# Kernel optimization log

Measured on AMD Instinct MI355X. Metric: run time of the kernel, lower is better.

Reference implementation:

```python
import jax, jax.numpy as jnp
import numpy as np

EMBED_DIM = 1280
NUM_HEADS = 20
HEAD_DIM = EMBED_DIM // NUM_HEADS
ENC_LEN = 8192
SCALE = float(HEAD_DIM ** -0.5)


def setup_inputs() -> dict:
    key = jax.random.key(0)
    ks = jax.random.split(key, 7)
    s = 0.02
    return {
        "hidden_states": jax.random.normal(ks[0], (1, 1, EMBED_DIM), dtype=jnp.float32),
        "cross_k_cache": jax.random.normal(ks[1], (1, NUM_HEADS, ENC_LEN, HEAD_DIM), dtype=jnp.float32),
        "cross_v_cache": jax.random.normal(ks[2], (1, NUM_HEADS, ENC_LEN, HEAD_DIM), dtype=jnp.float32),
        "q_w": jax.random.normal(ks[3], (EMBED_DIM, EMBED_DIM), dtype=jnp.float32) * s,
        "q_b": jax.random.normal(ks[4], (EMBED_DIM,), dtype=jnp.float32) * s,
        "out_w": jax.random.normal(ks[5], (EMBED_DIM, EMBED_DIM), dtype=jnp.float32) * s,
        "out_b": jax.random.normal(ks[6], (EMBED_DIM,), dtype=jnp.float32) * s,
    }


def reference(hidden_states, cross_k_cache, cross_v_cache, q_w, q_b, out_w, out_b):
    # q_proj (torch Linear: x @ W.T + b), then scale
    q = hidden_states @ q_w.T + q_b                       # [1,1,E]
    q = q * jnp.asarray(SCALE, q.dtype)
    q = q.reshape(1, 1, NUM_HEADS, HEAD_DIM).transpose(0, 2, 1, 3)  # [1,H,1,Dh]
    # attention scores over cached keys: [1,H,1,L]
    attn = jnp.einsum("bhqd,bhld->bhql", q, cross_k_cache)
    attn = jax.nn.softmax(attn, axis=-1)
    # weighted sum of values: [1,H,1,Dh]
    out = jnp.einsum("bhql,bhld->bhqd", attn, cross_v_cache)
    out = out.transpose(0, 2, 1, 3).reshape(1, 1, EMBED_DIM)
    return out @ out_w.T + out_b
```

## Files before the change

kernel.cpp:

```cpp
#include <hip/hip_runtime.h>
#include <math.h>

#define EMBED 1280
#define NHEAD 20
#define HDIM 64
#define LENC 8192
#define CHUNK 128
#define NCHUNK (LENC / CHUNK)
#define PREC 72
#define QSCALE 0.125f

__global__ __launch_bounds__(256) void matvec1280(
    const float* __restrict__ W, const float* __restrict__ x,
    const float* __restrict__ b, float* __restrict__ y, float scale) {
  int j = blockIdx.x * 4 + (threadIdx.x >> 6);
  int lane = threadIdx.x & 63;
  const float4* Wr = reinterpret_cast<const float4*>(W + (size_t)j * EMBED);
  const float4* x4 = reinterpret_cast<const float4*>(x);
  float acc = 0.f;
#pragma unroll
  for (int k = 0; k < 5; ++k) {
    float4 wv = Wr[lane + 64 * k];
    float4 xv = x4[lane + 64 * k];
    acc += wv.x * xv.x + wv.y * xv.y + wv.z * xv.z + wv.w * xv.w;
  }
#pragma unroll
  for (int m = 32; m > 0; m >>= 1) acc += __shfl_xor(acc, m);
  if (lane == 0) y[j] = scale * (acc + b[j]);
}

__global__ __launch_bounds__(256) void attn_partial(
    const float* __restrict__ K, const float* __restrict__ V,
    const float* __restrict__ q, float* __restrict__ part) {
  int blk = blockIdx.x;
  int h = blk / NCHUNK;
  int c = blk % NCHUNK;
  int tid = threadIdx.x;
  int w = tid >> 6;
  int lane = tid & 63;
  int grp = lane >> 4;
  int l16 = lane & 15;

  __shared__ float sc[CHUNK];
  __shared__ float red[8];
  __shared__ float4 ovec[4][16];

  const float4* Kh4 = reinterpret_cast<const float4*>(
      K + (size_t)h * LENC * HDIM + (size_t)c * CHUNK * HDIM);
  const float4* Vh4 = reinterpret_cast<const float4*>(
      V + (size_t)h * LENC * HDIM + (size_t)c * CHUNK * HDIM);
  float4 qv = reinterpret_cast<const float4*>(q + h * HDIM)[l16];

#pragma unroll
  for (int it = 0; it < CHUNK / 16; ++it) {
    int row = w * (CHUNK / 4) + it * 4 + grp;
    float4 kv = Kh4[row * 16 + l16];
    float s = kv.x * qv.x + kv.y * qv.y + kv.z * qv.z + kv.w * qv.w;
    s += __shfl_xor(s, 1);
    s += __shfl_xor(s, 2);
    s += __shfl_xor(s, 4);
    s += __shfl_xor(s, 8);
    if (l16 == 0) sc[row] = s;
  }
  __syncthreads();

  float m = (tid < CHUNK) ? sc[tid] : -INFINITY;
#pragma unroll
  for (int msk = 32; msk > 0; msk >>= 1) m = fmaxf(m, __shfl_xor(m, msk));
  if (lane == 0) red[w] = m;
  __syncthreads();
  float M = fmaxf(fmaxf(red[0], red[1]), fmaxf(red[2], red[3]));

  float e = (tid < CHUNK) ? expf(sc[tid] - M) : 0.f;
  if (tid < CHUNK) sc[tid] = e;
  float ssum = e;
#pragma unroll
  for (int msk = 32; msk > 0; msk >>= 1) ssum += __shfl_xor(ssum, msk);
  if (lane == 0) red[4 + w] = ssum;
  __syncthreads();
  float S = red[4] + red[5] + red[6] + red[7];

  float4 acc = make_float4(0.f, 0.f, 0.f, 0.f);
#pragma unroll
  for (int it = 0; it < CHUNK / 16; ++it) {
    int row = w * (CHUNK / 4) + it * 4 + grp;
    float4 vv = Vh4[row * 16 + l16];
    float p = sc[row];
    acc.x += p * vv.x; acc.y += p * vv.y; acc.z += p * vv.z; acc.w += p * vv.w;
  }
#pragma unroll
  for (int msk = 16; msk <= 32; msk <<= 1) {
    acc.x += __shfl_xor(acc.x, msk);
    acc.y += __shfl_xor(acc.y, msk);
    acc.z += __shfl_xor(acc.z, msk);
    acc.w += __shfl_xor(acc.w, msk);
  }
  if (grp == 0) ovec[w][l16] = acc;
  __syncthreads();

  if (w == 0 && grp == 0) {
    float4 o0 = ovec[0][l16], o1 = ovec[1][l16], o2 = ovec[2][l16], o3 = ovec[3][l16];
    float4 o = make_float4(o0.x + o1.x + o2.x + o3.x, o0.y + o1.y + o2.y + o3.y,
                           o0.z + o1.z + o2.z + o3.z, o0.w + o1.w + o2.w + o3.w);
    float* p = part + (size_t)(h * NCHUNK + c) * PREC;
    if (tid == 0) { p[0] = M; p[1] = S; }
    reinterpret_cast<float4*>(p + 4)[l16] = o;
  }
}

__global__ __launch_bounds__(64) void attn_combine(
    const float* __restrict__ part, float* __restrict__ attn_out) {
  int h = blockIdx.x;
  int lane = threadIdx.x;
  const float* p = part + (size_t)h * NCHUNK * PREC;
  float M = -INFINITY;
#pragma unroll
  for (int c = 0; c < NCHUNK; ++c) M = fmaxf(M, p[c * PREC]);
  float S = 0.f, o = 0.f;
#pragma unroll
  for (int c = 0; c < NCHUNK; ++c) {
    float f = expf(p[c * PREC] - M);
    S += p[c * PREC + 1] * f;
    o += p[c * PREC + 4 + lane] * f;
  }
  attn_out[h * HDIM + lane] = o / S;
}


extern "C" void kernel_launch(void* const* d_in, const int* in_sizes, int n_in,
                              void* d_out, int out_size, void* d_ws, size_t ws_size,
                              hipStream_t stream) {
  const float* hs    = (const float*)d_in[0];
  const float* Kc    = (const float*)d_in[1];
  const float* Vc    = (const float*)d_in[2];
  const float* q_w   = (const float*)d_in[3];
  const float* q_b   = (const float*)d_in[4];
  const float* out_w = (const float*)d_in[5];
  const float* out_b = (const float*)d_in[6];
  float* out = (float*)d_out;

  float* ws = (float*)d_ws;
  float* qv       = ws;
  float* attn_out = ws + EMBED;
  float* part     = ws + 2 * EMBED;

  matvec1280<<<EMBED / 4, 256, 0, stream>>>(q_w, hs, q_b, qv, QSCALE);
  attn_partial<<<NHEAD * NCHUNK, 256, 0, stream>>>(Kc, Vc, qv, part);
  attn_combine<<<NHEAD, 64, 0, stream>>>(part, attn_out);
  matvec1280<<<EMBED / 4, 256, 0, stream>>>(out_w, attn_out, out_b, out, 1.0f);
}
```

Before: 34.39 us.

## Fuse split-softmax combine into attention kernel via last-block atomic counter

Removes the separate combine kernel launch. Each attention block bumps a per-head atomic counter after writing its partial result, and the last block to finish for a head merges all the partials. The counters are zeroed inside the first matvec kernel. The matvec is also restructured to one row per 256-thread block (1280 blocks) with a shared-memory reduction, in place of four rows per block. The price is an atomic and fences per attention block, plus a serialized combine in the final block of each head.

```diff
diff --git a/kernel.cpp b/kernel.cpp
--- a/kernel.cpp
+++ b/kernel.cpp
@@ -10,28 +10,36 @@
 #define PREC 72
 #define QSCALE 0.125f
 
-__global__ __launch_bounds__(256) void matvec1280(
+__global__ __launch_bounds__(256) void matvec_row(
     const float* __restrict__ W, const float* __restrict__ x,
-    const float* __restrict__ b, float* __restrict__ y, float scale) {
-  int j = blockIdx.x * 4 + (threadIdx.x >> 6);
-  int lane = threadIdx.x & 63;
-  const float4* Wr = reinterpret_cast<const float4*>(W + (size_t)j * EMBED);
+    const float* __restrict__ b, float* __restrict__ y, float scale,
+    int* __restrict__ cnt_zero) {
+  if (cnt_zero != nullptr && blockIdx.x < NHEAD && threadIdx.x == 0)
+    __hip_atomic_store(&cnt_zero[blockIdx.x], 0, __ATOMIC_RELEASE,
+                       __HIP_MEMORY_SCOPE_AGENT);
+  int row = blockIdx.x;
+  int t = threadIdx.x;
+  int w = t >> 6, lane = t & 63;
+  const float4* Wr = reinterpret_cast<const float4*>(W + (size_t)row * EMBED);
   const float4* x4 = reinterpret_cast<const float4*>(x);
-  float acc = 0.f;
-#pragma unroll
-  for (int k = 0; k < 5; ++k) {
-    float4 wv = Wr[lane + 64 * k];
-    float4 xv = x4[lane + 64 * k];
-    acc += wv.x * xv.x + wv.y * xv.y + wv.z * xv.z + wv.w * xv.w;
+  float4 wv = Wr[t], xv = x4[t];
+  float acc = wv.x * xv.x + wv.y * xv.y + wv.z * xv.z + wv.w * xv.w;
+  if (t < 64) {
+    float4 wv2 = Wr[256 + t], xv2 = x4[256 + t];
+    acc += wv2.x * xv2.x + wv2.y * xv2.y + wv2.z * xv2.z + wv2.w * xv2.w;
   }
 #pragma unroll
-  for (int m = 32; m > 0; m >>= 1) acc += __shfl_xor(acc, m);
-  if (lane == 0) y[j] = scale * (acc + b[j]);
+  for (int msk = 32; msk > 0; msk >>= 1) acc += __shfl_xor(acc, msk);
+  __shared__ float red[4];
+  if (lane == 0) red[w] = acc;
+  __syncthreads();
+  if (t == 0) y[row] = scale * (red[0] + red[1] + red[2] + red[3] + b[row]);
 }
 
 __global__ __launch_bounds__(256) void attn_partial(
     const float* __restrict__ K, const float* __restrict__ V,
-    const float* __restrict__ q, float* __restrict__ part) {
+    const float* __restrict__ q, float* __restrict__ part,
+    int* __restrict__ cnt, float* __restrict__ attn_out) {
   int blk = blockIdx.x;
   int h = blk / NCHUNK;
   int c = blk % NCHUNK;
@@ -44,6 +52,7 @@
   __shared__ float sc[CHUNK];
   __shared__ float red[8];
   __shared__ float4 ovec[4][16];
+  __shared__ int sWon;
 
   const float4* Kh4 = reinterpret_cast<const float4*>(
       K + (size_t)h * LENC * HDIM + (size_t)c * CHUNK * HDIM);
@@ -106,24 +115,31 @@
     if (tid == 0) { p[0] = M; p[1] = S; }
     reinterpret_cast<float4*>(p + 4)[l16] = o;
   }
-}
+  __syncthreads();
 
-__global__ __launch_bounds__(64) void attn_combine(
-    const float* __restrict__ part, float* __restrict__ attn_out) {
-  int h = blockIdx.x;
-  int lane = threadIdx.x;
-  const float* p = part + (size_t)h * NCHUNK * PREC;
-  float M = -INFINITY;
+  if (tid == 0) {
+    __threadfence();
+    int old = atomicAdd(&cnt[h], 1);
+    sWon = (old == NCHUNK - 1) ? 1 : 0;
+  }
+  __syncthreads();
+  if (sWon) {
+    __threadfence();
+    if (tid < HDIM) {
+      const float* p = part + (size_t)h * NCHUNK * PREC;
+      float Mg = -INFINITY;
 #pragma unroll
-  for (int c = 0; c < NCHUNK; ++c) M = fmaxf(M, p[c * PREC]);
-  float S = 0.f, o = 0.f;
+      for (int cc = 0; cc < NCHUNK; ++cc) Mg = fmaxf(Mg, p[cc * PREC]);
+      float Sg = 0.f, o = 0.f;
 #pragma unroll
-  for (int c = 0; c < NCHUNK; ++c) {
-    float f = expf(p[c * PREC] - M);
-    S += p[c * PREC + 1] * f;
-    o += p[c * PREC + 4 + lane] * f;
+      for (int cc = 0; cc < NCHUNK; ++cc) {
+        float f = expf(p[cc * PREC] - Mg);
+        Sg += p[cc * PREC + 1] * f;
+        o += p[cc * PREC + 4 + tid] * f;
+      }
+      attn_out[h * HDIM + tid] = o / Sg;
+    }
   }
-  attn_out[h * HDIM + lane] = o / S;
 }
 
 
@@ -140,12 +156,12 @@
   float* out = (float*)d_out;
 
   float* ws = (float*)d_ws;
-  float* qv       = ws;
-  float* attn_out = ws + EMBED;
-  float* part     = ws + 2 * EMBED;
+  int*   cnt      = (int*)ws;
+  float* qv       = ws + 32;
+  float* attn_out = ws + 32 + EMBED;
+  float* part     = ws + 32 + 2 * EMBED;
 
-  matvec1280<<<EMBED / 4, 256, 0, stream>>>(q_w, hs, q_b, qv, QSCALE);
-  attn_partial<<<NHEAD * NCHUNK, 256, 0, stream>>>(Kc, Vc, qv, part);
-  attn_combine<<<NHEAD, 64, 0, stream>>>(part, attn_out);
-  matvec1280<<<EMBED / 4, 256, 0, stream>>>(out_w, attn_out, out_b, out, 1.0f);
+  matvec_row<<<EMBED, 256, 0, stream>>>(q_w, hs, q_b, qv, QSCALE, cnt);
+  attn_partial<<<NHEAD * NCHUNK, 256, 0, stream>>>(Kc, Vc, qv, part, cnt, attn_out);
+  matvec_row<<<EMBED, 256, 0, stream>>>(out_w, attn_out, out_b, out, 1.0f, nullptr);
 }
```

Measured after the change: 83.14 us. +141.7%, slower.

## Make attention partials wave-local, preload K/V in registers, parallelize combine

Applied to the files above, without the earlier changes.

The attention partial kernel now has each wavefront do its own 32-row softmax. Each wavefront writes its own partial record (256 records per head), so the block-wide shared-memory reductions and syncthreads are gone. All K and V loads are issued up front into registers to raise memory-level parallelism. The combine kernel uses 256 threads with shared-memory reductions over four times as many records, and the matvec now assigns one row per 256-thread block. The trade-offs are more partial-record traffic, more register pressure, and four times more matvec blocks.

```diff
diff --git a/kernel.cpp b/kernel.cpp
--- a/kernel.cpp
+++ b/kernel.cpp
@@ -6,124 +6,143 @@
 #define HDIM 64
 #define LENC 8192
 #define CHUNK 128
-#define NCHUNK (LENC / CHUNK)
+#define NBLK (LENC / CHUNK)
+#define NREC 256
 #define PREC 72
 #define QSCALE 0.125f
 
-__global__ __launch_bounds__(256) void matvec1280(
+__global__ __launch_bounds__(256) void matvec_row(
     const float* __restrict__ W, const float* __restrict__ x,
     const float* __restrict__ b, float* __restrict__ y, float scale) {
-  int j = blockIdx.x * 4 + (threadIdx.x >> 6);
-  int lane = threadIdx.x & 63;
-  const float4* Wr = reinterpret_cast<const float4*>(W + (size_t)j * EMBED);
+  int row = blockIdx.x;
+  int t = threadIdx.x;
+  int w = t >> 6, lane = t & 63;
+  const float4* Wr = reinterpret_cast<const float4*>(W + (size_t)row * EMBED);
   const float4* x4 = reinterpret_cast<const float4*>(x);
-  float acc = 0.f;
-#pragma unroll
-  for (int k = 0; k < 5; ++k) {
-    float4 wv = Wr[lane + 64 * k];
-    float4 xv = x4[lane + 64 * k];
-    acc += wv.x * xv.x + wv.y * xv.y + wv.z * xv.z + wv.w * xv.w;
+  float4 wv = Wr[t], xv = x4[t];
+  float acc = wv.x * xv.x + wv.y * xv.y + wv.z * xv.z + wv.w * xv.w;
+  if (t < 64) {
+    float4 wv2 = Wr[256 + t], xv2 = x4[256 + t];
+    acc += wv2.x * xv2.x + wv2.y * xv2.y + wv2.z * xv2.z + wv2.w * xv2.w;
   }
 #pragma unroll
-  for (int m = 32; m > 0; m >>= 1) acc += __shfl_xor(acc, m);
-  if (lane == 0) y[j] = scale * (acc + b[j]);
+  for (int msk = 32; msk > 0; msk >>= 1) acc += __shfl_xor(acc, msk);
+  __shared__ float red[4];
+  if (lane == 0) red[w] = acc;
+  __syncthreads();
+  if (t == 0) y[row] = scale * (red[0] + red[1] + red[2] + red[3] + b[row]);
 }
 
 __global__ __launch_bounds__(256) void attn_partial(
     const float* __restrict__ K, const float* __restrict__ V,
     const float* __restrict__ q, float* __restrict__ part) {
   int blk = blockIdx.x;
-  int h = blk / NCHUNK;
-  int c = blk % NCHUNK;
+  int h = blk / NBLK;
+  int c = blk % NBLK;
   int tid = threadIdx.x;
   int w = tid >> 6;
   int lane = tid & 63;
   int grp = lane >> 4;
   int l16 = lane & 15;
 
-  __shared__ float sc[CHUNK];
-  __shared__ float red[8];
-  __shared__ float4 ovec[4][16];
-
-  const float4* Kh4 = reinterpret_cast<const float4*>(
-      K + (size_t)h * LENC * HDIM + (size_t)c * CHUNK * HDIM);
-  const float4* Vh4 = reinterpret_cast<const float4*>(
-      V + (size_t)h * LENC * HDIM + (size_t)c * CHUNK * HDIM);
+  size_t row0 = (size_t)c * CHUNK + (size_t)w * 32;
+  const float4* Kh4 = reinterpret_cast<const float4*>(K + (size_t)h * LENC * HDIM) + row0 * 16;
+  const float4* Vh4 = reinterpret_cast<const float4*>(V + (size_t)h * LENC * HDIM) + row0 * 16;
   float4 qv = reinterpret_cast<const float4*>(q + h * HDIM)[l16];
 
+  float4 kreg[8], vreg[8];
 #pragma unroll
-  for (int it = 0; it < CHUNK / 16; ++it) {
-    int row = w * (CHUNK / 4) + it * 4 + grp;
-    float4 kv = Kh4[row * 16 + l16];
-    float s = kv.x * qv.x + kv.y * qv.y + kv.z * qv.z + kv.w * qv.w;
-    s += __shfl_xor(s, 1);
-    s += __shfl_xor(s, 2);
-    s += __shfl_xor(s, 4);
-    s += __shfl_xor(s, 8);
-    if (l16 == 0) sc[row] = s;
+  for (int it = 0; it < 8; ++it) kreg[it] = Kh4[(it * 4 + grp) * 16 + l16];
+#pragma unroll
+  for (int it = 0; it < 8; ++it) vreg[it] = Vh4[(it * 4 + grp) * 16 + l16];
+
+  float s[8];
+#pragma unroll
+  for (int it = 0; it < 8; ++it) {
+    float t = kreg[it].x * qv.x + kreg[it].y * qv.y + kreg[it].z * qv.z + kreg[it].w * qv.w;
+    t += __shfl_xor(t, 1);
+    t += __shfl_xor(t, 2);
+    t += __shfl_xor(t, 4);
+    t += __shfl_xor(t, 8);
+    s[it] = t;
   }
-  __syncthreads();
 
-  float m = (tid < CHUNK) ? sc[tid] : -INFINITY;
+  float m = s[0];
 #pragma unroll
-  for (int msk = 32; msk > 0; msk >>= 1) m = fmaxf(m, __shfl_xor(m, msk));
-  if (lane == 0) red[w] = m;
-  __syncthreads();
-  float M = fmaxf(fmaxf(red[0], red[1]), fmaxf(red[2], red[3]));
+  for (int it = 1; it < 8; ++it) m = fmaxf(m, s[it]);
+  m = fmaxf(m, __shfl_xor(m, 16));
+  m = fmaxf(m, __shfl_xor(m, 32));
 
-  float e = (tid < CHUNK) ? expf(sc[tid] - M) : 0.f;
-  if (tid < CHUNK) sc[tid] = e;
-  float ssum = e;
+  float e[8], ssum = 0.f;
 #pragma unroll
-  for (int msk = 32; msk > 0; msk >>= 1) ssum += __shfl_xor(ssum, msk);
-  if (lane == 0) red[4 + w] = ssum;
-  __syncthreads();
-  float S = red[4] + red[5] + red[6] + red[7];
+  for (int it = 0; it < 8; ++it) { e[it] = expf(s[it] - m); ssum += e[it]; }
+  ssum += __shfl_xor(ssum, 16);
+  ssum += __shfl_xor(ssum, 32);
 
-  float4 acc = make_float4(0.f, 0.f, 0.f, 0.f);
+  float4 o = make_float4(0.f, 0.f, 0.f, 0.f);
 #pragma unroll
-  for (int it = 0; it < CHUNK / 16; ++it) {
-    int row = w * (CHUNK / 4) + it * 4 + grp;
-    float4 vv = Vh4[row * 16 + l16];
-    float p = sc[row];
-    acc.x += p * vv.x; acc.y += p * vv.y; acc.z += p * vv.z; acc.w += p * vv.w;
+  for (int it = 0; it < 8; ++it) {
+    o.x += e[it] * vreg[it].x;
+    o.y += e[it] * vreg[it].y;
+    o.z += e[it] * vreg[it].z;
+    o.w += e[it] * vreg[it].w;
   }
 #pragma unroll
   for (int msk = 16; msk <= 32; msk <<= 1) {
-    acc.x += __shfl_xor(acc.x, msk);
-    acc.y += __shfl_xor(acc.y, msk);
-    acc.z += __shfl_xor(acc.z, msk);
-    acc.w += __shfl_xor(acc.w, msk);
+    o.x += __shfl_xor(o.x, msk);
+    o.y += __shfl_xor(o.y, msk);
+    o.z += __shfl_xor(o.z, msk);
+    o.w += __shfl_xor(o.w, msk);
   }
-  if (grp == 0) ovec[w][l16] = acc;
-  __syncthreads();
 
-  if (w == 0 && grp == 0) {
-    float4 o0 = ovec[0][l16], o1 = ovec[1][l16], o2 = ovec[2][l16], o3 = ovec[3][l16];
-    float4 o = make_float4(o0.x + o1.x + o2.x + o3.x, o0.y + o1.y + o2.y + o3.y,
-                           o0.z + o1.z + o2.z + o3.z, o0.w + o1.w + o2.w + o3.w);
-    float* p = part + (size_t)(h * NCHUNK + c) * PREC;
-    if (tid == 0) { p[0] = M; p[1] = S; }
+  float* p = part + (size_t)(h * NREC + c * 4 + w) * PREC;
+  if (grp == 0) {
+    if (l16 == 0) { p[0] = m; p[1] = ssum; }
     reinterpret_cast<float4*>(p + 4)[l16] = o;
   }
 }
 
-__global__ __launch_bounds__(64) void attn_combine(
+__global__ __launch_bounds__(256) void attn_combine(
     const float* __restrict__ part, float* __restrict__ attn_out) {
   int h = blockIdx.x;
-  int lane = threadIdx.x;
-  const float* p = part + (size_t)h * NCHUNK * PREC;
-  float M = -INFINITY;
+  int tid = threadIdx.x;
+  int w = tid >> 6, lane = tid & 63;
+  const float* p = part + (size_t)h * NREC * PREC;
+
+  __shared__ float fsh[NREC];
+  __shared__ float redM[4], redS[4];
+  __shared__ float osum[4][HDIM];
+
+  float mt = p[tid * PREC];
+  float st = p[tid * PREC + 1];
+  float m = mt;
 #pragma unroll
-  for (int c = 0; c < NCHUNK; ++c) M = fmaxf(M, p[c * PREC]);
-  float S = 0.f, o = 0.f;
+  for (int msk = 32; msk > 0; msk >>= 1) m = fmaxf(m, __shfl_xor(m, msk));
+  if (lane == 0) redM[w] = m;
+  __syncthreads();
+  float Mg = fmaxf(fmaxf(redM[0], redM[1]), fmaxf(redM[2], redM[3]));
+
+  float f = expf(mt - Mg);
+  fsh[tid] = f;
+  float sc = st * f;
 #pragma unroll
-  for (int c = 0; c < NCHUNK; ++c) {
-    float f = expf(p[c * PREC] - M);
-    S += p[c * PREC + 1] * f;
-    o += p[c * PREC + 4 + lane] * f;
+  for (int msk = 32; msk > 0; msk >>= 1) sc += __shfl_xor(sc, msk);
+  if (lane == 0) redS[w] = sc;
+  __syncthreads();
+  float Sg = redS[0] + redS[1] + redS[2] + redS[3];
+
+  float o = 0.f;
+#pragma unroll
+  for (int r = 0; r < 64; ++r) {
+    int rec = w * 64 + r;
+    o += fsh[rec] * p[rec * PREC + 4 + lane];
   }
-  attn_out[h * HDIM + lane] = o / S;
+  osum[w][lane] = o;
+  __syncthreads();
+  if (w == 0) {
+    float oo = osum[0][lane] + osum[1][lane] + osum[2][lane] + osum[3][lane];
+    attn_out[h * HDIM + lane] = oo / Sg;
+  }
 }
 
 
@@ -144,8 +163,8 @@
   float* attn_out = ws + EMBED;
   float* part     = ws + 2 * EMBED;
 
-  matvec1280<<<EMBED / 4, 256, 0, stream>>>(q_w, hs, q_b, qv, QSCALE);
-  attn_partial<<<NHEAD * NCHUNK, 256, 0, stream>>>(Kc, Vc, qv, part);
-  attn_combine<<<NHEAD, 64, 0, stream>>>(part, attn_out);
-  matvec1280<<<EMBED / 4, 256, 0, stream>>>(out_w, attn_out, out_b, out, 1.0f);
+  matvec_row<<<EMBED, 256, 0, stream>>>(q_w, hs, q_b, qv, QSCALE);
+  attn_partial<<<NHEAD * NBLK, 256, 0, stream>>>(Kc, Vc, qv, part);
+  attn_combine<<<NHEAD, 256, 0, stream>>>(part, attn_out);
+  matvec_row<<<EMBED, 256, 0, stream>>>(out_w, attn_out, out_b, out, 1.0f);
 }
```

After: 29.30 us. 1.17x faster.
